# Kernel tuning notes

Hardware: AMD Instinct MI355X
Metric: run time of the kernel (lower is better)

## Reference

```python
import jax, jax.numpy as jnp
import numpy as np
from jax import lax

T, B, D = 200, 1024, 128  # max_len, batch, units (= input feature dim)


def setup_inputs() -> dict:
    key = jax.random.key(0)
    ks = jax.random.split(key, 16)
    s = 1.0 / np.sqrt(D)
    inp = {
        "inputs": jax.random.normal(ks[0], (T, B, D), dtype=jnp.float32),
        "state": jnp.zeros((B, D), dtype=jnp.float32),
        "att_score": jax.random.uniform(ks[1], (T, B, 1), dtype=jnp.float32),
        # binary validity mask [B, T], float because it multiplies the state
        "mask": (jax.random.uniform(ks[2], (B, T)) < 0.9).astype(jnp.float32),
        "max_len": T,
        # u gate (Bilinear: Dense(a) with bias + Dense(b) no bias)
        "Wau": jax.random.normal(ks[3], (D, D), dtype=jnp.float32) * s,
        "bau": jnp.zeros((D,), dtype=jnp.float32),
        "Wbu": jax.random.normal(ks[4], (D, D), dtype=jnp.float32) * s,
        # r gate
        "War": jax.random.normal(ks[5], (D, D), dtype=jnp.float32) * s,
        "bar": jnp.zeros((D,), dtype=jnp.float32),
        "Wbr": jax.random.normal(ks[6], (D, D), dtype=jnp.float32) * s,
        # candidate memory
        "Wac": jax.random.normal(ks[7], (D, D), dtype=jnp.float32) * s,
        "bac": jnp.zeros((D,), dtype=jnp.float32),
        "Wbc": jax.random.normal(ks[8], (D, D), dtype=jnp.float32) * s,
    }
    return inp


def reference(inputs, state, att_score, mask, max_len,
              Wau, bau, Wbu, War, bar, Wbr, Wac, bac, Wbc):
    # time-major mask [T, B, 1]
    mask_t = jnp.swapaxes(mask, 0, 1)[:, :, None]

    def step(s, xs):
        x, a, m = xs  # x:[B,D], a:[B,1], m:[B,1]
        u = jax.nn.sigmoid(x @ Wau + bau + s @ Wbu)
        r = jax.nn.sigmoid(x @ War + bar + s @ Wbr)
        c = jnp.tanh(x @ Wac + bac + r * (s @ Wbc))
        u_ = a * u
        new = (1.0 - u_) * s + u_ * c
        s = new * m + s * (1.0 - m)
        return s, None

    final_state, _ = lax.scan(step, state, (inputs, att_score, mask_t))
    return final_state
```

## Files before the change

### kernel.cpp

```cpp
#include <hip/hip_runtime.h>
#include <stdint.h>

#define T_LEN 200
#define B_SZ  1024
#define D_DIM 128
#define LOG2E 1.44269504088896340736f

typedef __bf16 bf16_t;
typedef __bf16 bf16x8 __attribute__((ext_vector_type(8)));
typedef float  f32x4  __attribute__((ext_vector_type(4)));

union BF8 { bf16x8 v; bf16_t e[8]; };

__device__ inline uint32_t pk_bf16(float a, float b) {
  uint32_t ua = __float_as_uint(a), ub = __float_as_uint(b);
  ua += 0x7fffu + ((ua >> 16) & 1u);
  ub += 0x7fffu + ((ub >> 16) & 1u);
  return (ua >> 16) | (ub & 0xffff0000u);
}
__device__ inline float rcp_f(float x) { return __builtin_amdgcn_rcpf(x); }

#define BAR_LDS() asm volatile("s_waitcnt lgkmcnt(0)\n\ts_barrier" ::: "memory")

__global__ __launch_bounds__(512, 2) void augru_fused(
    const float* __restrict__ x,
    const float* __restrict__ state,
    const float* __restrict__ att,
    const float* __restrict__ mask,
    const float* __restrict__ Wau, const float* __restrict__ bau,
    const float* __restrict__ Wbu,
    const float* __restrict__ War, const float* __restrict__ bar,
    const float* __restrict__ Wbr,
    const float* __restrict__ Wac, const float* __restrict__ bac,
    const float* __restrict__ Wbc,
    float* __restrict__ out)
{
  __shared__ bf16_t xb[2][2048];
  __shared__ bf16_t sb[2][2048];
  __shared__ float  am_lds[T_LEN * 16];

  const int tid = threadIdx.x;
  const int w  = tid >> 6;
  const int l  = tid & 63;
  const int lm = l & 15;
  const int lg = l >> 4;
  const int bb = blockIdx.x;
  const int R0 = bb * 16;
  const int col = w * 16 + lm;

  BF8 xu[4], xr[4], xc[4];
  BF8 su[4], sr[4], sc[4];
#pragma unroll
  for (int kk = 0; kk < 4; ++kk) {
#pragma unroll
    for (int j = 0; j < 8; ++j) {
      int k = kk * 32 + lg * 8 + j;
      xu[kk].e[j] = (bf16_t)(Wau[k * 128 + col] * LOG2E);
      xr[kk].e[j] = (bf16_t)(War[k * 128 + col] * LOG2E);
      xc[kk].e[j] = (bf16_t)(Wac[k * 128 + col] * (2.0f * LOG2E));
      su[kk].e[j] = (bf16_t)(Wbu[k * 128 + col] * LOG2E);
      sr[kk].e[j] = (bf16_t)(Wbr[k * 128 + col] * LOG2E);
      sc[kk].e[j] = (bf16_t)(Wbc[k * 128 + col] * (2.0f * LOG2E));
    }
  }
  const float b_u = bau[col] * LOG2E;
  const float b_r = bar[col] * LOG2E;
  const float b_c = bac[col] * (2.0f * LOG2E);

  for (int idx = tid; idx < T_LEN * 16; idx += 512) {
    int t = idx >> 4, row = idx & 15;
    am_lds[idx] = att[t * B_SZ + R0 + row] * mask[(R0 + row) * T_LEN + t];
  }

  float sreg[4];
#pragma unroll
  for (int i = 0; i < 4; ++i)
    sreg[i] = state[(R0 + lg * 4 + i) * 128 + col];

  for (int idx = tid; idx < 2048; idx += 512) {
    int row = idx >> 7, k = idx & 127;
    sb[0][(k >> 3) * 128 + (row ^ (2 * ((k >> 3) & 1))) * 8 + (k & 7)] =
        (bf16_t)state[(R0 + row) * 128 + k];
  }

  const int srow = tid & 15;
  const int sc4  = tid >> 4;
  const int stg_pos = (sc4 >> 1) * 128 + srow * 8 + (sc4 & 1) * 4;
  const float* xrow = x + (size_t)(R0 + srow) * 128 + sc4 * 4;
  const size_t xstep = (size_t)B_SZ * 128;

  {
    float4 v0 = *(const float4*)(xrow);
    float4 v1 = *(const float4*)(xrow + xstep);
    uint2 p0; p0.x = pk_bf16(v0.x, v0.y); p0.y = pk_bf16(v0.z, v0.w);
    uint2 p1; p1.x = pk_bf16(v1.x, v1.y); p1.y = pk_bf16(v1.z, v1.w);
    *(uint2*)&xb[0][stg_pos] = p0;
    *(uint2*)&xb[1][stg_pos] = p1;
  }
  float4 xq0 = *(const float4*)(xrow + 2 * xstep);
  float4 xq1 = *(const float4*)(xrow + 3 * xstep);
  float4 xq2 = *(const float4*)(xrow + 4 * xstep);

  __syncthreads();

  f32x4 gU = {b_u, b_u, b_u, b_u};
  f32x4 gR = {b_r, b_r, b_r, b_r};
  f32x4 gC = {b_c, b_c, b_c, b_c};
  {
    bf16x8 ax[4];
#pragma unroll
    for (int kk = 0; kk < 4; ++kk)
      ax[kk] = *(const bf16x8*)&xb[0][kk * 512 + 8 * l];
#pragma unroll
    for (int kk = 0; kk < 4; ++kk) {
      gU = __builtin_amdgcn_mfma_f32_16x16x32_bf16(ax[kk], xu[kk].v, gU, 0, 0, 0);
      gR = __builtin_amdgcn_mfma_f32_16x16x32_bf16(ax[kk], xr[kk].v, gR, 0, 0, 0);
      gC = __builtin_amdgcn_mfma_f32_16x16x32_bf16(ax[kk], xc[kk].v, gC, 0, 0, 0);
    }
  }
  union F4 { float4 v; float e[4]; } amv;
  amv.v = *(const float4*)&am_lds[lg * 4];

  const int lx8   = 8 * (l ^ (2 * (lg & 1)));
  const int psi   = 2 * ((col >> 3) & 1);
  const int wbase = (col >> 3) * 128 + lg * 32 + (col & 7);

  BAR_LDS();

  auto step = [&](int t) {
    const int rp = t & 1;

    {
      uint2 p; p.x = pk_bf16(xq0.x, xq0.y); p.y = pk_bf16(xq0.z, xq0.w);
      *(uint2*)&xb[rp][stg_pos] = p;
    }
    xq0 = xq1; xq1 = xq2;
    int tl = t + 5; if (tl > T_LEN - 1) tl = T_LEN - 1;
    xq2 = *(const float4*)(xrow + (size_t)tl * xstep);

    bf16x8 ax[4], as_[4];
#pragma unroll
    for (int kk = 0; kk < 4; ++kk) {
      ax[kk]  = *(const bf16x8*)&xb[rp ^ 1][kk * 512 + 8 * l];
      as_[kk] = *(const bf16x8*)&sb[rp][kk * 512 + lx8];
    }

    f32x4 aU = gU, aR = gR;
    f32x4 bC = {0.f, 0.f, 0.f, 0.f};
    f32x4 nU = {b_u, b_u, b_u, b_u};
    f32x4 nR = {b_r, b_r, b_r, b_r};
    f32x4 nC = {b_c, b_c, b_c, b_c};
#pragma unroll
    for (int kk = 0; kk < 4; ++kk) {
      aU = __builtin_amdgcn_mfma_f32_16x16x32_bf16(as_[kk], su[kk].v, aU, 0, 0, 0);
      nU = __builtin_amdgcn_mfma_f32_16x16x32_bf16(ax[kk],  xu[kk].v, nU, 0, 0, 0);
      aR = __builtin_amdgcn_mfma_f32_16x16x32_bf16(as_[kk], sr[kk].v, aR, 0, 0, 0);
      nR = __builtin_amdgcn_mfma_f32_16x16x32_bf16(ax[kk],  xr[kk].v, nR, 0, 0, 0);
      bC = __builtin_amdgcn_mfma_f32_16x16x32_bf16(as_[kk], sc[kk].v, bC, 0, 0, 0);
      nC = __builtin_amdgcn_mfma_f32_16x16x32_bf16(ax[kk],  xc[kk].v, nC, 0, 0, 0);
    }

    bf16_t* wbuf = sb[rp ^ 1];
#pragma unroll
    for (int i = 0; i < 4; ++i) {
      float u  = rcp_f(1.0f + __builtin_amdgcn_exp2f(-aU[i]));
      float r  = rcp_f(1.0f + __builtin_amdgcn_exp2f(-aR[i]));
      float wc = fmaf(r, bC[i], gC[i]);
      float cg = fmaf(-2.0f, rcp_f(__builtin_amdgcn_exp2f(wc) + 1.0f), 1.0f);
      float sf = fmaf(amv.e[i] * u, cg - sreg[i], sreg[i]);
      sreg[i] = sf;
      wbuf[wbase + 8 * (i ^ psi)] = (bf16_t)sf;
    }

    gU = nU; gR = nR; gC = nC;
    int ta = t + 1; if (ta > T_LEN - 1) ta = T_LEN - 1;
    amv.v = *(const float4*)&am_lds[ta * 16 + lg * 4];

    BAR_LDS();
  };

#pragma unroll 1
  for (int t = 0; t < T_LEN; t += 2) {
    step(t);
    step(t + 1);
  }

#pragma unroll
  for (int i = 0; i < 4; ++i)
    out[(R0 + lg * 4 + i) * 128 + col] = sreg[i];
}

extern "C" void kernel_launch(void* const* d_in, const int* in_sizes, int n_in,
                              void* d_out, int out_size, void* d_ws, size_t ws_size,
                              hipStream_t stream)
{
  const float* x    = (const float*)d_in[0];
  const float* st   = (const float*)d_in[1];
  const float* att  = (const float*)d_in[2];
  const float* mask = (const float*)d_in[3];
  const float* Wau  = (const float*)d_in[5];
  const float* bau  = (const float*)d_in[6];
  const float* Wbu  = (const float*)d_in[7];
  const float* War  = (const float*)d_in[8];
  const float* bar  = (const float*)d_in[9];
  const float* Wbr  = (const float*)d_in[10];
  const float* Wac  = (const float*)d_in[11];
  const float* bac  = (const float*)d_in[12];
  const float* Wbc  = (const float*)d_in[13];

  (void)d_ws; (void)ws_size;

  augru_fused<<<dim3(64), dim3(512), 0, stream>>>(
      x, st, att, mask, Wau, bau, Wbu, War, bar, Wbr, Wac, bac, Wbc,
      (float*)d_out);
}
```

Baseline: 309.2 us.

## Halve waves per block, give each wave two column tiles, reorder recurrent MFMAs first

Each block now runs 4 waves instead of 8, and each wave owns 32 output columns (two 16-wide MFMA tiles), so it holds twice the weight fragments in registers. The step issues the state-dependent MFMAs before loading x and computing the next step's input projection, and moves x staging after the gate math. The aim is to shorten the serial critical path per timestep and make barriers cheaper with fewer waves. The cost is more per-wave work and register pressure, which could lengthen each step.

```diff
diff --git a/kernel.cpp b/kernel.cpp
--- a/kernel.cpp
+++ b/kernel.cpp
@@ -22,7 +22,7 @@
 
 #define BAR_LDS() asm volatile("s_waitcnt lgkmcnt(0)\n\ts_barrier" ::: "memory")
 
-__global__ __launch_bounds__(512, 2) void augru_fused(
+__global__ __launch_bounds__(256, 1) void augru_fused(
     const float* __restrict__ x,
     const float* __restrict__ state,
     const float* __restrict__ att,
@@ -46,133 +46,174 @@
   const int lg = l >> 4;
   const int bb = blockIdx.x;
   const int R0 = bb * 16;
-  const int col = w * 16 + lm;
-
-  BF8 xu[4], xr[4], xc[4];
-  BF8 su[4], sr[4], sc[4];
-#pragma unroll
-  for (int kk = 0; kk < 4; ++kk) {
-#pragma unroll
-    for (int j = 0; j < 8; ++j) {
-      int k = kk * 32 + lg * 8 + j;
-      xu[kk].e[j] = (bf16_t)(Wau[k * 128 + col] * LOG2E);
-      xr[kk].e[j] = (bf16_t)(War[k * 128 + col] * LOG2E);
-      xc[kk].e[j] = (bf16_t)(Wac[k * 128 + col] * (2.0f * LOG2E));
-      su[kk].e[j] = (bf16_t)(Wbu[k * 128 + col] * LOG2E);
-      sr[kk].e[j] = (bf16_t)(Wbr[k * 128 + col] * LOG2E);
-      sc[kk].e[j] = (bf16_t)(Wbc[k * 128 + col] * (2.0f * LOG2E));
+  const int col0 = w * 32 + lm;
+
+  BF8 xu[2][4], xr[2][4], xc[2][4];
+  BF8 su[2][4], sr[2][4], sc[2][4];
+  float b_u[2], b_r[2], b_c[2];
+#pragma unroll
+  for (int j = 0; j < 2; ++j) {
+    const int cj = col0 + 16 * j;
+#pragma unroll
+    for (int kk = 0; kk < 4; ++kk) {
+#pragma unroll
+      for (int e = 0; e < 8; ++e) {
+        int k = kk * 32 + lg * 8 + e;
+        xu[j][kk].e[e] = (bf16_t)(Wau[k * 128 + cj] * LOG2E);
+        xr[j][kk].e[e] = (bf16_t)(War[k * 128 + cj] * LOG2E);
+        xc[j][kk].e[e] = (bf16_t)(Wac[k * 128 + cj] * (2.0f * LOG2E));
+        su[j][kk].e[e] = (bf16_t)(Wbu[k * 128 + cj] * LOG2E);
+        sr[j][kk].e[e] = (bf16_t)(Wbr[k * 128 + cj] * LOG2E);
+        sc[j][kk].e[e] = (bf16_t)(Wbc[k * 128 + cj] * (2.0f * LOG2E));
+      }
     }
-  }
-  const float b_u = bau[col] * LOG2E;
-  const float b_r = bar[col] * LOG2E;
-  const float b_c = bac[col] * (2.0f * LOG2E);
-
-  for (int idx = tid; idx < T_LEN * 16; idx += 512) {
+    b_u[j] = bau[cj] * LOG2E;
+    b_r[j] = bar[cj] * LOG2E;
+    b_c[j] = bac[cj] * (2.0f * LOG2E);
+  }
+
+  for (int idx = tid; idx < T_LEN * 16; idx += 256) {
     int t = idx >> 4, row = idx & 15;
     am_lds[idx] = att[t * B_SZ + R0 + row] * mask[(R0 + row) * T_LEN + t];
   }
 
-  float sreg[4];
-#pragma unroll
-  for (int i = 0; i < 4; ++i)
-    sreg[i] = state[(R0 + lg * 4 + i) * 128 + col];
-
-  for (int idx = tid; idx < 2048; idx += 512) {
+  float sreg[2][4];
+#pragma unroll
+  for (int j = 0; j < 2; ++j)
+#pragma unroll
+    for (int i = 0; i < 4; ++i)
+      sreg[j][i] = state[(R0 + lg * 4 + i) * 128 + col0 + 16 * j];
+
+  for (int idx = tid; idx < 2048; idx += 256) {
     int row = idx >> 7, k = idx & 127;
     sb[0][(k >> 3) * 128 + (row ^ (2 * ((k >> 3) & 1))) * 8 + (k & 7)] =
         (bf16_t)state[(R0 + row) * 128 + k];
   }
 
   const int srow = tid & 15;
-  const int sc4  = tid >> 4;
-  const int stg_pos = (sc4 >> 1) * 128 + srow * 8 + (sc4 & 1) * 4;
-  const float* xrow = x + (size_t)(R0 + srow) * 128 + sc4 * 4;
+  const int sm   = tid >> 4;
+  const int stg_pos = sm * 128 + srow * 8;
+  const float* xrow = x + (size_t)(R0 + srow) * 128 + sm * 8;
   const size_t xstep = (size_t)B_SZ * 128;
 
+  auto stage = [&](float4 a, float4 b, int buf) {
+    uint4 p;
+    p.x = pk_bf16(a.x, a.y); p.y = pk_bf16(a.z, a.w);
+    p.z = pk_bf16(b.x, b.y); p.w = pk_bf16(b.z, b.w);
+    *(uint4*)&xb[buf][stg_pos] = p;
+  };
+
   {
-    float4 v0 = *(const float4*)(xrow);
-    float4 v1 = *(const float4*)(xrow + xstep);
-    uint2 p0; p0.x = pk_bf16(v0.x, v0.y); p0.y = pk_bf16(v0.z, v0.w);
-    uint2 p1; p1.x = pk_bf16(v1.x, v1.y); p1.y = pk_bf16(v1.z, v1.w);
-    *(uint2*)&xb[0][stg_pos] = p0;
-    *(uint2*)&xb[1][stg_pos] = p1;
-  }
-  float4 xq0 = *(const float4*)(xrow + 2 * xstep);
-  float4 xq1 = *(const float4*)(xrow + 3 * xstep);
-  float4 xq2 = *(const float4*)(xrow + 4 * xstep);
+    float4 a0 = *(const float4*)(xrow);
+    float4 b0 = *(const float4*)(xrow + 4);
+    float4 a1 = *(const float4*)(xrow + xstep);
+    float4 b1 = *(const float4*)(xrow + xstep + 4);
+    stage(a0, b0, 0);
+    stage(a1, b1, 1);
+  }
+  float4 xqa0 = *(const float4*)(xrow + 2 * xstep);
+  float4 xqb0 = *(const float4*)(xrow + 2 * xstep + 4);
+  float4 xqa1 = *(const float4*)(xrow + 3 * xstep);
+  float4 xqb1 = *(const float4*)(xrow + 3 * xstep + 4);
+  float4 xqa2 = *(const float4*)(xrow + 4 * xstep);
+  float4 xqb2 = *(const float4*)(xrow + 4 * xstep + 4);
 
   __syncthreads();
 
-  f32x4 gU = {b_u, b_u, b_u, b_u};
-  f32x4 gR = {b_r, b_r, b_r, b_r};
-  f32x4 gC = {b_c, b_c, b_c, b_c};
+  f32x4 gU[2], gR[2], gC[2];
+#pragma unroll
+  for (int j = 0; j < 2; ++j) {
+    gU[j] = f32x4{b_u[j], b_u[j], b_u[j], b_u[j]};
+    gR[j] = f32x4{b_r[j], b_r[j], b_r[j], b_r[j]};
+    gC[j] = f32x4{b_c[j], b_c[j], b_c[j], b_c[j]};
+  }
   {
     bf16x8 ax[4];
 #pragma unroll
     for (int kk = 0; kk < 4; ++kk)
       ax[kk] = *(const bf16x8*)&xb[0][kk * 512 + 8 * l];
 #pragma unroll
-    for (int kk = 0; kk < 4; ++kk) {
-      gU = __builtin_amdgcn_mfma_f32_16x16x32_bf16(ax[kk], xu[kk].v, gU, 0, 0, 0);
-      gR = __builtin_amdgcn_mfma_f32_16x16x32_bf16(ax[kk], xr[kk].v, gR, 0, 0, 0);
-      gC = __builtin_amdgcn_mfma_f32_16x16x32_bf16(ax[kk], xc[kk].v, gC, 0, 0, 0);
-    }
+    for (int kk = 0; kk < 4; ++kk)
+#pragma unroll
+      for (int j = 0; j < 2; ++j) {
+        gU[j] = __builtin_amdgcn_mfma_f32_16x16x32_bf16(ax[kk], xu[j][kk].v, gU[j], 0, 0, 0);
+        gR[j] = __builtin_amdgcn_mfma_f32_16x16x32_bf16(ax[kk], xr[j][kk].v, gR[j], 0, 0, 0);
+        gC[j] = __builtin_amdgcn_mfma_f32_16x16x32_bf16(ax[kk], xc[j][kk].v, gC[j], 0, 0, 0);
+      }
   }
   union F4 { float4 v; float e[4]; } amv;
   amv.v = *(const float4*)&am_lds[lg * 4];
 
   const int lx8   = 8 * (l ^ (2 * (lg & 1)));
-  const int psi   = 2 * ((col >> 3) & 1);
-  const int wbase = (col >> 3) * 128 + lg * 32 + (col & 7);
+  const int psi   = 2 * ((col0 >> 3) & 1);
+  const int wbase = (col0 >> 3) * 128 + lg * 32 + (col0 & 7);
 
   BAR_LDS();
 
   auto step = [&](int t) {
     const int rp = t & 1;
 
-    {
-      uint2 p; p.x = pk_bf16(xq0.x, xq0.y); p.y = pk_bf16(xq0.z, xq0.w);
-      *(uint2*)&xb[rp][stg_pos] = p;
+    bf16x8 as_[4];
+#pragma unroll
+    for (int kk = 0; kk < 4; ++kk)
+      as_[kk] = *(const bf16x8*)&sb[rp][kk * 512 + lx8];
+
+    f32x4 aU[2] = {gU[0], gU[1]};
+    f32x4 aR[2] = {gR[0], gR[1]};
+    f32x4 bC[2] = {f32x4{0,0,0,0}, f32x4{0,0,0,0}};
+#pragma unroll
+    for (int kk = 0; kk < 4; ++kk)
+#pragma unroll
+      for (int j = 0; j < 2; ++j) {
+        aU[j] = __builtin_amdgcn_mfma_f32_16x16x32_bf16(as_[kk], su[j][kk].v, aU[j], 0, 0, 0);
+        aR[j] = __builtin_amdgcn_mfma_f32_16x16x32_bf16(as_[kk], sr[j][kk].v, aR[j], 0, 0, 0);
+        bC[j] = __builtin_amdgcn_mfma_f32_16x16x32_bf16(as_[kk], sc[j][kk].v, bC[j], 0, 0, 0);
+      }
+
+    bf16x8 ax[4];
+#pragma unroll
+    for (int kk = 0; kk < 4; ++kk)
+      ax[kk] = *(const bf16x8*)&xb[rp ^ 1][kk * 512 + 8 * l];
+
+    f32x4 nU[2], nR[2], nC[2];
+#pragma unroll
+    for (int j = 0; j < 2; ++j) {
+      nU[j] = f32x4{b_u[j], b_u[j], b_u[j], b_u[j]};
+      nR[j] = f32x4{b_r[j], b_r[j], b_r[j], b_r[j]};
+      nC[j] = f32x4{b_c[j], b_c[j], b_c[j], b_c[j]};
     }
-    xq0 = xq1; xq1 = xq2;
+#pragma unroll
+    for (int kk = 0; kk < 4; ++kk)
+#pragma unroll
+      for (int j = 0; j < 2; ++j) {
+        nU[j] = __builtin_amdgcn_mfma_f32_16x16x32_bf16(ax[kk], xu[j][kk].v, nU[j], 0, 0, 0);
+        nR[j] = __builtin_amdgcn_mfma_f32_16x16x32_bf16(ax[kk], xr[j][kk].v, nR[j], 0, 0, 0);
+        nC[j] = __builtin_amdgcn_mfma_f32_16x16x32_bf16(ax[kk], xc[j][kk].v, nC[j], 0, 0, 0);
+      }
+
+    bf16_t* wbuf = sb[rp ^ 1];
+#pragma unroll
+    for (int j = 0; j < 2; ++j)
+#pragma unroll
+      for (int i = 0; i < 4; ++i) {
+        float u  = rcp_f(1.0f + __builtin_amdgcn_exp2f(-aU[j][i]));
+        float r  = rcp_f(1.0f + __builtin_amdgcn_exp2f(-aR[j][i]));
+        float wc = fmaf(r, bC[j][i], gC[j][i]);
+        float cg = fmaf(-2.0f, rcp_f(__builtin_amdgcn_exp2f(wc) + 1.0f), 1.0f);
+        float sf = fmaf(amv.e[i] * u, cg - sreg[j][i], sreg[j][i]);
+        sreg[j][i] = sf;
+        wbuf[wbase + j * 256 + 8 * (i ^ psi)] = (bf16_t)sf;
+      }
+
+    stage(xqa0, xqb0, rp);
+    xqa0 = xqa1; xqb0 = xqb1;
+    xqa1 = xqa2; xqb1 = xqb2;
     int tl = t + 5; if (tl > T_LEN - 1) tl = T_LEN - 1;
-    xq2 = *(const float4*)(xrow + (size_t)tl * xstep);
-
-    bf16x8 ax[4], as_[4];
-#pragma unroll
-    for (int kk = 0; kk < 4; ++kk) {
-      ax[kk]  = *(const bf16x8*)&xb[rp ^ 1][kk * 512 + 8 * l];
-      as_[kk] = *(const bf16x8*)&sb[rp][kk * 512 + lx8];
-    }
-
-    f32x4 aU = gU, aR = gR;
-    f32x4 bC = {0.f, 0.f, 0.f, 0.f};
-    f32x4 nU = {b_u, b_u, b_u, b_u};
-    f32x4 nR = {b_r, b_r, b_r, b_r};
-    f32x4 nC = {b_c, b_c, b_c, b_c};
-#pragma unroll
-    for (int kk = 0; kk < 4; ++kk) {
-      aU = __builtin_amdgcn_mfma_f32_16x16x32_bf16(as_[kk], su[kk].v, aU, 0, 0, 0);
-      nU = __builtin_amdgcn_mfma_f32_16x16x32_bf16(ax[kk],  xu[kk].v, nU, 0, 0, 0);
-      aR = __builtin_amdgcn_mfma_f32_16x16x32_bf16(as_[kk], sr[kk].v, aR, 0, 0, 0);
-      nR = __builtin_amdgcn_mfma_f32_16x16x32_bf16(ax[kk],  xr[kk].v, nR, 0, 0, 0);
-      bC = __builtin_amdgcn_mfma_f32_16x16x32_bf16(as_[kk], sc[kk].v, bC, 0, 0, 0);
-      nC = __builtin_amdgcn_mfma_f32_16x16x32_bf16(ax[kk],  xc[kk].v, nC, 0, 0, 0);
-    }
-
-    bf16_t* wbuf = sb[rp ^ 1];
-#pragma unroll
-    for (int i = 0; i < 4; ++i) {
-      float u  = rcp_f(1.0f + __builtin_amdgcn_exp2f(-aU[i]));
-      float r  = rcp_f(1.0f + __builtin_amdgcn_exp2f(-aR[i]));
-      float wc = fmaf(r, bC[i], gC[i]);
-      float cg = fmaf(-2.0f, rcp_f(__builtin_amdgcn_exp2f(wc) + 1.0f), 1.0f);
-      float sf = fmaf(amv.e[i] * u, cg - sreg[i], sreg[i]);
-      sreg[i] = sf;
-      wbuf[wbase + 8 * (i ^ psi)] = (bf16_t)sf;
-    }
-
-    gU = nU; gR = nR; gC = nC;
+    xqa2 = *(const float4*)(xrow + (size_t)tl * xstep);
+    xqb2 = *(const float4*)(xrow + (size_t)tl * xstep + 4);
+
+#pragma unroll
+    for (int j = 0; j < 2; ++j) { gU[j] = nU[j]; gR[j] = nR[j]; gC[j] = nC[j]; }
     int ta = t + 1; if (ta > T_LEN - 1) ta = T_LEN - 1;
     amv.v = *(const float4*)&am_lds[ta * 16 + lg * 4];
 
@@ -186,8 +227,10 @@
   }
 
 #pragma unroll
-  for (int i = 0; i < 4; ++i)
-    out[(R0 + lg * 4 + i) * 128 + col] = sreg[i];
+  for (int j = 0; j < 2; ++j)
+#pragma unroll
+    for (int i = 0; i < 4; ++i)
+      out[(R0 + lg * 4 + i) * 128 + col0 + 16 * j] = sreg[j][i];
 }
 
 extern "C" void kernel_launch(void* const* d_in, const int* in_sizes, int n_in,
@@ -210,7 +253,7 @@
 
   (void)d_ws; (void)ws_size;
 
-  augru_fused<<<dim3(64), dim3(512), 0, stream>>>(
+  augru_fused<<<dim3(64), dim3(256), 0, stream>>>(
       x, st, att, mask, Wau, bau, Wbu, War, bar, Wbr, Wac, bac, Wbc,
       (float*)d_out);
 }
```

After: 335.6 us. 1.09x slower.
